# Kernel tuning notes

Hardware: AMD Instinct MI355X
Metric: run time of the kernel (lower is better)

Reference implementation:

```python
import jax, jax.numpy as jnp
import numpy as np

N = 4
IS_SLOW = (False, False, True, True)
RATES = (1, 1, 4, 4)
THRESH = 0.3
F2S_IDX = {(0, 2): 0, (0, 3): 1, (1, 2): 2, (1, 3): 3}


def _conv1d(x, w, stride, pad):
    # x: [B, C_in, T], w: [C_out, C_in, K]
    return jax.lax.conv_general_dilated(
        x, w, (stride,), [(pad, pad)], dimension_numbers=("NCH", "OIH", "NCH"))


def _linear_interp(x, t_out):
    # x: [B, D, T_in] -> [B, D, t_out]; matches F.interpolate(mode='linear', align_corners=False)
    t_in = x.shape[2]
    scale = t_in / t_out
    src = (jnp.arange(t_out, dtype=jnp.float32) + 0.5) * scale - 0.5
    src = jnp.clip(src, 0.0, float(t_in - 1))
    i0 = jnp.floor(src).astype(jnp.int32)
    i1 = jnp.minimum(i0 + 1, t_in - 1)
    w = (src - i0.astype(jnp.float32)).astype(x.dtype)
    return x[:, :, i0] * (1.0 - w) + x[:, :, i1] * w


def setup_inputs() -> dict:
    key = jax.random.key(0)
    ks = jax.random.split(key, 8)
    T_FAST, T_SLOW, B, D, H = 512, 128, 32, 1024, 256
    return {
        "feat0": jax.random.normal(ks[0], (T_FAST, B, D), jnp.float32),
        "feat1": jax.random.normal(ks[1], (T_FAST, B, D), jnp.float32),
        "feat2": jax.random.normal(ks[2], (T_SLOW, B, D), jnp.float32),
        "feat3": jax.random.normal(ks[3], (T_SLOW, B, D), jnp.float32),
        "mlp_w1": jax.random.normal(ks[4], (N * N, 2 * D, H), jnp.float32) * 0.02,
        "mlp_b1": jnp.zeros((N * N, H), jnp.float32),
        "mlp_w2": jax.random.normal(ks[5], (N * N, H, 1), jnp.float32) * 0.02,
        "mlp_b2": jnp.zeros((N * N, 1), jnp.float32),
        "s2f_w": jax.random.normal(ks[6], (D, D, 1), jnp.float32) * 0.02,
        "s2f_b": jnp.zeros((D,), jnp.float32),
        "f2s_w": jax.random.normal(ks[7], (4, D, D, 5), jnp.float32) * 0.02,
    }


def reference(feat0, feat1, feat2, feat3, mlp_w1, mlp_b1, mlp_w2, mlp_b2,
              s2f_w, s2f_b, f2s_w):
    feats = [feat0, feat1, feat2, feat3]            # [T_i, B, D]
    feats_bdt = [jnp.transpose(f, (1, 2, 0)) for f in feats]  # [B, D, T_i]
    globals_ = [f.mean(axis=2) for f in feats_bdt]  # [B, D]
    outputs = list(feats)
    for i in range(N):
        for j in range(N):
            if i == j:
                continue
            p = i * N + j
            pair_vec = jnp.concatenate([globals_[i], globals_[j]], axis=-1)  # [B, 2D]
            h = jax.nn.relu(pair_vec @ mlp_w1[p] + mlp_b1[p])
            score = jax.nn.sigmoid(h @ mlp_w2[p] + mlp_b2[p])[:, 0]          # [B]
            cond = score.mean() >= THRESH
            if IS_SLOW[i] and not IS_SLOW[j]:
                # slow -> fast: interpolate up, 1x1 conv proj, score-weighted residual
                up = _linear_interp(feats_bdt[i], feats_bdt[j].shape[2])
                up = _conv1d(up, s2f_w, 1, 0) + s2f_b[None, :, None]
                new = feats_bdt[j] + score[:, None, None] * up
                outputs[j] = jnp.where(cond, jnp.transpose(new, (2, 0, 1)), outputs[j])
            elif (not IS_SLOW[i]) and IS_SLOW[j]:
                # fast -> slow: strided conv down, score-weighted residual
                stride = RATES[j] // RATES[i]
                down = _conv1d(feats_bdt[i], f2s_w[F2S_IDX[(i, j)]], stride, 2)
                new = feats_bdt[j] + score[:, None, None] * down
                outputs[j] = jnp.where(cond, jnp.transpose(new, (2, 0, 1)), outputs[j])
    return tuple(outputs)
```

## Files before the change

### kernel.cpp

```cpp
#include <hip/hip_runtime.h>
#include <math.h>
#include <stdint.h>

typedef __bf16 bf16;
typedef bf16 bf16x8 __attribute__((ext_vector_type(8)));
typedef bf16 bf16x4 __attribute__((ext_vector_type(4)));
typedef float f32x4 __attribute__((ext_vector_type(4)));

#define OFF_GLOB   0ul
#define OFF_H      524288ul
#define OFF_SCORE  786432ul
#define OFF_COND   787456ul
#define OFF_PART   788480ul
#define OFF_PROJ   4982784ul
#define OFF_WTF2S  38537216ul
#define OFF_WTS2F  59508736ul
#define OFF_F0B    61605888ul
#define OFF_F1B    95160320ul
#define OFF_F2B    128714752ul
#define OFF_F3B    137103360ul
#define WS_NEED    145491968ul

__device__ __forceinline__ void gl2lds16(const void* g, void* lds) {
  __builtin_amdgcn_global_load_lds(
      (const __attribute__((address_space(1))) unsigned int*)g,
      (__attribute__((address_space(3))) unsigned int*)lds, 16, 0, 0);
}

__device__ __forceinline__ void slot_ij(int s, int& i, int& j) {
  if (s < 4) { i = 2 + (s & 1); j = s >> 1; }
  else       { int ss = s - 4; i = ss & 1; j = 2 + (ss >> 1); }
}

__global__ __launch_bounds__(256) void k_means_part(
    const float* __restrict__ f0, const float* __restrict__ f1,
    const float* __restrict__ f2, const float* __restrict__ f3,
    float* __restrict__ part,
    bf16* __restrict__ b0, bf16* __restrict__ b1,
    bf16* __restrict__ b2, bf16* __restrict__ b3, int do_conv)
{
  int b = blockIdx.x, c = blockIdx.y, i = blockIdx.z, tid = threadIdx.x;
  const float* f = (i == 0) ? f0 : (i == 1) ? f1 : (i == 2) ? f2 : f3;
  bf16* fb = (i == 0) ? b0 : (i == 1) ? b1 : (i == 2) ? b2 : b3;
  int chunk = (i < 2) ? 64 : 16;
  int t0 = c * chunk;
  float4 s = make_float4(0.f, 0.f, 0.f, 0.f);
  for (int t = t0; t < t0 + chunk; ++t) {
    float4 v = ((const float4*)(f + (size_t)(t * 32 + b) * 1024))[tid];
    s.x += v.x; s.y += v.y; s.z += v.z; s.w += v.w;
    if (do_conv) {
      bf16x4 o;
      o[0] = (bf16)v.x; o[1] = (bf16)v.y; o[2] = (bf16)v.z; o[3] = (bf16)v.w;
      *(bf16x4*)(fb + (size_t)(t * 32 + b) * 1024 + tid * 4) = o;
    }
  }
  ((float4*)part)[(size_t)((i * 8 + c) * 32 + b) * 256 + tid] = s;
}

__global__ __launch_bounds__(256) void k_means_final(
    const float* __restrict__ part, float* __restrict__ g)
{
  int b = blockIdx.x, i = blockIdx.y, tid = threadIdx.x;
  float4 s = make_float4(0.f, 0.f, 0.f, 0.f);
  for (int c = 0; c < 8; ++c) {
    float4 v = ((const float4*)part)[(size_t)((i * 8 + c) * 32 + b) * 256 + tid];
    s.x += v.x; s.y += v.y; s.z += v.z; s.w += v.w;
  }
  float inv = (i < 2) ? (1.f / 512.f) : (1.f / 128.f);
  s.x *= inv; s.y *= inv; s.z *= inv; s.w *= inv;
  ((float4*)g)[(size_t)(i * 32 + b) * 256 + tid] = s;
}

__global__ __launch_bounds__(256) void k_mlp1(
    const float* __restrict__ g, const float* __restrict__ w1, float* __restrict__ h_ws)
{
  int s = blockIdx.x, hc = blockIdx.y, kz = blockIdx.z, tid = threadIdx.x;
  int pi, pj; slot_ij(s, pi, pj);
  int p = pi * 4 + pj;
  int h = hc * 32 + (tid & 31);
  int bg = tid >> 5;
  __shared__ float pv[32 * 65];
  float acc0 = 0.f, acc1 = 0.f, acc2 = 0.f, acc3 = 0.f;
  for (int kt = 0; kt < 8; ++kt) {
    int k0 = kz * 512 + kt * 64;
    __syncthreads();
    for (int l = tid; l < 2048; l += 256) {
      int bb = l >> 6, kk = l & 63;
      int k = k0 + kk;
      float v = (k < 1024) ? g[(size_t)pi * 32768 + bb * 1024 + k]
                           : g[(size_t)pj * 32768 + bb * 1024 + (k - 1024)];
      pv[bb * 65 + kk] = v;
    }
    __syncthreads();
    const float* wp = w1 + ((size_t)p * 2048 + k0) * 256 + hc * 32 + (tid & 31);
    for (int kk = 0; kk < 64; ++kk) {
      float w = wp[(size_t)kk * 256];
      acc0 += pv[(bg * 4 + 0) * 65 + kk] * w;
      acc1 += pv[(bg * 4 + 1) * 65 + kk] * w;
      acc2 += pv[(bg * 4 + 2) * 65 + kk] * w;
      acc3 += pv[(bg * 4 + 3) * 65 + kk] * w;
    }
  }
  atomicAdd(&h_ws[(size_t)s * 8192 + (bg * 4 + 0) * 256 + h], acc0);
  atomicAdd(&h_ws[(size_t)s * 8192 + (bg * 4 + 1) * 256 + h], acc1);
  atomicAdd(&h_ws[(size_t)s * 8192 + (bg * 4 + 2) * 256 + h], acc2);
  atomicAdd(&h_ws[(size_t)s * 8192 + (bg * 4 + 3) * 256 + h], acc3);
}

__global__ __launch_bounds__(256) void k_mlp2(
    const float* __restrict__ h_ws, const float* __restrict__ b1,
    const float* __restrict__ w2, const float* __restrict__ b2,
    float* __restrict__ score, float* __restrict__ cond)
{
  int s = blockIdx.x, tid = threadIdx.x;
  int pi, pj; slot_ij(s, pi, pj);
  int p = pi * 4 + pj;
  int lane = tid & 63, wv = tid >> 6;
  float4 w2v = ((const float4*)(w2 + p * 256))[lane];
  float4 b1v = ((const float4*)(b1 + p * 256))[lane];
  float b2v = b2[p];
  __shared__ float redw[4];
  float tot = 0.f;
  for (int bb = 0; bb < 8; ++bb) {
    int b = wv * 8 + bb;
    float4 h4 = ((const float4*)(h_ws + (size_t)s * 8192 + b * 256))[lane];
    float v = fmaxf(h4.x + b1v.x, 0.f) * w2v.x + fmaxf(h4.y + b1v.y, 0.f) * w2v.y
            + fmaxf(h4.z + b1v.z, 0.f) * w2v.z + fmaxf(h4.w + b1v.w, 0.f) * w2v.w;
    #pragma unroll
    for (int off = 32; off > 0; off >>= 1) v += __shfl_down(v, off);
    if (lane == 0) {
      float sc = 1.f / (1.f + expf(-(v + b2v)));
      score[s * 32 + b] = sc;
      tot += sc;
    }
  }
  if (lane == 0) redw[wv] = tot;
  __syncthreads();
  if (tid == 0) {
    float t = redw[0] + redw[1] + redw[2] + redw[3];
    cond[s] = (t * (1.f / 32.f) >= 0.3f) ? 1.f : 0.f;
  }
}

__global__ __launch_bounds__(256) void k_f2s_transpose(
    const float* __restrict__ w, const float* __restrict__ cond, bf16* __restrict__ wT)
{
  int z = blockIdx.y, co = blockIdx.x, tid = threadIdx.x;
  int sel = (cond[5 + 2 * z] > 0.5f) ? 1 : ((cond[4 + 2 * z] > 0.5f) ? 0 : -1);
  if (sel < 0) return;
  int widx = sel * 2 + z;
  __shared__ float buf[5120];
  const float* src = w + ((size_t)widx * 1024 + co) * 5120;
  for (int l = tid; l < 5120; l += 256) buf[l] = src[l];
  __syncthreads();
  bf16* dst = wT + (size_t)z * 5242880 + (size_t)co * 5120;
  for (int o = tid; o < 5120; o += 256) {
    int kk = o >> 10, ci = o & 1023;
    dst[o] = (bf16)buf[ci * 5 + kk];
  }
}

__global__ __launch_bounds__(256) void k_s2f_convert(
    const float* __restrict__ w, bf16* __restrict__ wT)
{
  size_t gi = (size_t)blockIdx.x * 256 + threadIdx.x;
  float4 v = ((const float4*)w)[gi];
  bf16x4 o;
  o[0] = (bf16)v.x; o[1] = (bf16)v.y; o[2] = (bf16)v.z; o[3] = (bf16)v.w;
  *(bf16x4*)&wT[gi * 4] = o;
}


__global__ __launch_bounds__(256) void k_s2f_gemm2(
    const bf16* __restrict__ f2b, const bf16* __restrict__ f3b,
    const bf16* __restrict__ wT, const float* __restrict__ s2f_b,
    const float* __restrict__ cond, float* __restrict__ proj)
{
  int z = blockIdx.z;
  int sel = (cond[1 + 2 * z] > 0.5f) ? 3 : ((cond[2 * z] > 0.5f) ? 2 : -1);
  if (sel < 0) return;
  const bf16* Ab = (sel == 3) ? f3b : f2b;
  float* projz = proj + (size_t)z * 4194304;
  int tid = threadIdx.x;
  int lin = blockIdx.y * 32 + blockIdx.x;
  int o_ = (lin & 7) * 32 + (lin >> 3);
  int M0 = (o_ & 31) * 128, N0 = (o_ >> 5) * 128;
  __shared__ bf16 As[2][8192];
  __shared__ bf16 Bs[2][8192];
  f32x4 acc[4][4];
  #pragma unroll
  for (int a = 0; a < 4; ++a)
    #pragma unroll
    for (int c = 0; c < 4; ++c) { acc[a][c][0] = 0.f; acc[a][c][1] = 0.f; acc[a][c][2] = 0.f; acc[a][c][3] = 0.f; }
  int lane = tid & 63, wv = tid >> 6;
  int wr = (wv >> 1) * 64, wc = (wv & 1) * 64;
  int rl = lane & 15, q = lane >> 4;
  int wb = tid & 192;

  size_t aoffs[4], boffs[4];
  #pragma unroll
  for (int rnd = 0; rnd < 4; ++rnd) {
    int c = rnd * 256 + tid, lr = c >> 3, seg = c & 7, sw = seg ^ (lr & 7);
    aoffs[rnd] = (size_t)(M0 + lr) * 1024 + sw * 8;
    boffs[rnd] = (size_t)(N0 + lr) * 1024 + sw * 8;
  }

  #define S2F_STAGE(KT, PB) {                                        \
    size_t ci0 = (size_t)(KT) * 64;                                  \
    _Pragma("unroll")                                                \
    for (int rnd = 0; rnd < 4; ++rnd) {                              \
      gl2lds16(Ab + aoffs[rnd] + ci0, &As[PB][(rnd * 256 + wb) * 8]);\
      gl2lds16(wT + boffs[rnd] + ci0, &Bs[PB][(rnd * 256 + wb) * 8]);\
    } }

  S2F_STAGE(0, 0);
  __syncthreads();
  for (int kt = 0; kt < 16; ++kt) {
    int pb = kt & 1;
    if (kt < 15) S2F_STAGE(kt + 1, pb ^ 1);
    const bf16* Ac = &As[pb][0];
    const bf16* Bc = &Bs[pb][0];
    #pragma unroll
    for (int ks = 0; ks < 2; ++ks) {
      bf16x8 af[4], bfv[4];
      #pragma unroll
      for (int mi = 0; mi < 4; ++mi) {
        int r = wr + mi * 16 + rl;
        af[mi] = *(const bf16x8*)&Ac[r * 64 + (((ks << 2) + q) ^ (r & 7)) * 8];
      }
      #pragma unroll
      for (int ni = 0; ni < 4; ++ni) {
        int r = wc + ni * 16 + rl;
        bfv[ni] = *(const bf16x8*)&Bc[r * 64 + (((ks << 2) + q) ^ (r & 7)) * 8];
      }
      #pragma unroll
      for (int mi = 0; mi < 4; ++mi)
        #pragma unroll
        for (int ni = 0; ni < 4; ++ni)
          acc[mi][ni] = __builtin_amdgcn_mfma_f32_16x16x32_bf16(af[mi], bfv[ni], acc[mi][ni], 0, 0, 0);
    }
    __syncthreads();
  }
  #pragma unroll
  for (int mi = 0; mi < 4; ++mi)
    #pragma unroll
    for (int ni = 0; ni < 4; ++ni)
      #pragma unroll
      for (int r = 0; r < 4; ++r) {
        int gm = M0 + wr + mi * 16 + q * 4 + r;
        int gn = N0 + wc + ni * 16 + rl;
        projz[(size_t)gm * 1024 + gn] = acc[mi][ni][r] + s2f_b[gn];
      }
}

__global__ __launch_bounds__(256) void k_f2s_gemm2(
    const bf16* __restrict__ f0b, const bf16* __restrict__ f1b,
    const float* __restrict__ feat2, const float* __restrict__ feat3,
    const bf16* __restrict__ wT, const float* __restrict__ score,
    const float* __restrict__ cond, const bf16* __restrict__ zbuf,
    float* __restrict__ out)
{
  int z = blockIdx.z;
  const float* fj = z ? feat3 : feat2;
  float* oj = out + 33554432ul + (size_t)z * 4194304;
  int tid = threadIdx.x;
  int lin = blockIdx.y * 32 + blockIdx.x;
  int o_ = (lin & 7) * 32 + (lin >> 3);
  int M0 = (o_ & 31) * 128, N0 = (o_ >> 5) * 128;
  int sel = (cond[5 + 2 * z] > 0.5f) ? 1 : ((cond[4 + 2 * z] > 0.5f) ? 0 : -1);
  if (sel < 0) {
    for (int l = tid; l < 4096; l += 256) {
      int rr = l >> 5, c4 = l & 31;
      size_t idx = (size_t)(M0 + rr) * 1024 + N0 + c4 * 4;
      *(float4*)(oj + idx) = *(const float4*)(fj + idx);
    }
    return;
  }
  const bf16* Ab = sel ? f1b : f0b;
  const bf16* wTz = wT + (size_t)z * 5242880;
  int slot = (sel ? 5 : 4) + 2 * z;
  __shared__ bf16 As[2][8192];
  __shared__ bf16 Bs[2][8192];
  __shared__ float sld[32];
  if (tid < 32) sld[tid] = score[slot * 32 + tid];
  f32x4 acc[4][4];
  #pragma unroll
  for (int a = 0; a < 4; ++a)
    #pragma unroll
    for (int c = 0; c < 4; ++c) { acc[a][c][0] = 0.f; acc[a][c][1] = 0.f; acc[a][c][2] = 0.f; acc[a][c][3] = 0.f; }
  int lane = tid & 63, wv = tid >> 6;
  int wr = (wv >> 1) * 64, wc = (wv & 1) * 64;
  int rl = lane & 15, q = lane >> 4;
  int wb = tid & 192;

  long aoffs[4]; size_t boffs[4]; bool t0f[4];
  #pragma unroll
  for (int rnd = 0; rnd < 4; ++rnd) {
    int c = rnd * 256 + tid, lr = c >> 3, seg = c & 7, sw = seg ^ (lr & 7);
    int m = M0 + lr, t = m >> 5, b = m & 31;
    aoffs[rnd] = ((long)(4 * t - 2) * 32 + b) * 1024 + sw * 8;
    t0f[rnd] = (t == 0);
    boffs[rnd] = (size_t)(N0 + lr) * 5120 + sw * 8;
  }

  #define F2S_STAGE(KT, PB) {                                                   \
    int kk_ = (KT) >> 4;                                                        \
    long aadd_ = (long)kk_ * 32768 + (((KT) & 15) << 6);                        \
    size_t badd_ = (size_t)(KT) * 64;                                           \
    bool zk_ = (kk_ < 2);                                                       \
    _Pragma("unroll")                                                           \
    for (int rnd = 0; rnd < 4; ++rnd) {                                         \
      const bf16* sA = (zk_ && t0f[rnd]) ? zbuf : (Ab + aoffs[rnd] + aadd_);    \
      gl2lds16(sA, &As[PB][(rnd * 256 + wb) * 8]);                              \
      gl2lds16(wTz + boffs[rnd] + badd_, &Bs[PB][(rnd * 256 + wb) * 8]);        \
    } }

  F2S_STAGE(0, 0);
  __syncthreads();
  for (int kt = 0; kt < 80; ++kt) {
    int pb = kt & 1;
    if (kt < 79) F2S_STAGE(kt + 1, pb ^ 1);
    const bf16* Ac = &As[pb][0];
    const bf16* Bc = &Bs[pb][0];
    #pragma unroll
    for (int ks = 0; ks < 2; ++ks) {
      bf16x8 af[4], bfv[4];
      #pragma unroll
      for (int mi = 0; mi < 4; ++mi) {
        int r = wr + mi * 16 + rl;
        af[mi] = *(const bf16x8*)&Ac[r * 64 + (((ks << 2) + q) ^ (r & 7)) * 8];
      }
      #pragma unroll
      for (int ni = 0; ni < 4; ++ni) {
        int r = wc + ni * 16 + rl;
        bfv[ni] = *(const bf16x8*)&Bc[r * 64 + (((ks << 2) + q) ^ (r & 7)) * 8];
      }
      #pragma unroll
      for (int mi = 0; mi < 4; ++mi)
        #pragma unroll
        for (int ni = 0; ni < 4; ++ni)
          acc[mi][ni] = __builtin_amdgcn_mfma_f32_16x16x32_bf16(af[mi], bfv[ni], acc[mi][ni], 0, 0, 0);
    }
    __syncthreads();
  }
  #pragma unroll
  for (int mi = 0; mi < 4; ++mi)
    #pragma unroll
    for (int ni = 0; ni < 4; ++ni)
      #pragma unroll
      for (int r = 0; r < 4; ++r) {
        int gm = M0 + wr + mi * 16 + q * 4 + r;
        int gn = N0 + wc + ni * 16 + rl;
        size_t idx = (size_t)gm * 1024 + gn;
        oj[idx] = fj[idx] + sld[gm & 31] * acc[mi][ni][r];
      }
}

__global__ __launch_bounds__(256) void k_s2f_gemm_fb(
    const float* __restrict__ feat2, const float* __restrict__ feat3,
    const bf16* __restrict__ wT, const float* __restrict__ s2f_b,
    const float* __restrict__ cond, float* __restrict__ proj)
{
  int z = blockIdx.z;
  int sel = (cond[1 + 2 * z] > 0.5f) ? 3 : ((cond[2 * z] > 0.5f) ? 2 : -1);
  if (sel < 0) return;
  const float* A = (sel == 3) ? feat3 : feat2;
  float* projz = proj + (size_t)z * 4194304;
  int tid = threadIdx.x;
  int lin = blockIdx.y * 32 + blockIdx.x;
  int o_ = (lin & 7) * 32 + (lin >> 3);
  int M0 = (o_ & 31) * 128, N0 = (o_ >> 5) * 128;
  __shared__ bf16 As[128][72];
  __shared__ bf16 Bs[128][72];
  f32x4 acc[4][4];
  for (int a = 0; a < 4; ++a)
    for (int c = 0; c < 4; ++c) { acc[a][c][0] = 0.f; acc[a][c][1] = 0.f; acc[a][c][2] = 0.f; acc[a][c][3] = 0.f; }
  int row = tid >> 1, half = tid & 1;
  int lane = tid & 63, wv = tid >> 6;
  int wr = (wv >> 1) * 64, wc = (wv & 1) * 64;
  int rl = lane & 15, q = lane >> 4;
  for (int kt = 0; kt < 16; ++kt) {
    int ci0 = kt * 64;
    __syncthreads();
    {
      const float4* src = (const float4*)(A + (size_t)(M0 + row) * 1024 + ci0 + half * 32);
      #pragma unroll
      for (int u = 0; u < 4; ++u) {
        float4 v0 = src[2 * u], v1 = src[2 * u + 1];
        bf16x8 pk;
        pk[0] = (bf16)v0.x; pk[1] = (bf16)v0.y; pk[2] = (bf16)v0.z; pk[3] = (bf16)v0.w;
        pk[4] = (bf16)v1.x; pk[5] = (bf16)v1.y; pk[6] = (bf16)v1.z; pk[7] = (bf16)v1.w;
        *(bf16x8*)&As[row][half * 32 + u * 8] = pk;
      }
      const uint4* bs = (const uint4*)(wT + (size_t)(N0 + row) * 1024 + ci0 + half * 32);
      #pragma unroll
      for (int u = 0; u < 4; ++u) *(uint4*)&Bs[row][half * 32 + u * 8] = bs[u];
    }
    __syncthreads();
    #pragma unroll
    for (int ks = 0; ks < 2; ++ks) {
      bf16x8 af[4], bfv[4];
      #pragma unroll
      for (int mi = 0; mi < 4; ++mi) af[mi] = *(const bf16x8*)&As[wr + mi * 16 + rl][ks * 32 + q * 8];
      #pragma unroll
      for (int ni = 0; ni < 4; ++ni) bfv[ni] = *(const bf16x8*)&Bs[wc + ni * 16 + rl][ks * 32 + q * 8];
      #pragma unroll
      for (int mi = 0; mi < 4; ++mi)
        #pragma unroll
        for (int ni = 0; ni < 4; ++ni)
          acc[mi][ni] = __builtin_amdgcn_mfma_f32_16x16x32_bf16(af[mi], bfv[ni], acc[mi][ni], 0, 0, 0);
    }
  }
  #pragma unroll
  for (int mi = 0; mi < 4; ++mi)
    #pragma unroll
    for (int ni = 0; ni < 4; ++ni)
      #pragma unroll
      for (int r = 0; r < 4; ++r) {
        int gm = M0 + wr + mi * 16 + q * 4 + r;
        int gn = N0 + wc + ni * 16 + rl;
        projz[(size_t)gm * 1024 + gn] = acc[mi][ni][r] + s2f_b[gn];
      }
}

__global__ __launch_bounds__(256) void k_f2s_gemm_fb(
    const float* __restrict__ feat0, const float* __restrict__ feat1,
    const float* __restrict__ feat2, const float* __restrict__ feat3,
    const bf16* __restrict__ wT, const float* __restrict__ score,
    const float* __restrict__ cond, float* __restrict__ out)
{
  int z = blockIdx.z;
  const float* fj = z ? feat3 : feat2;
  float* oj = out + 33554432ul + (size_t)z * 4194304;
  int tid = threadIdx.x;
  int lin = blockIdx.y * 32 + blockIdx.x;
  int o_ = (lin & 7) * 32 + (lin >> 3);
  int M0 = (o_ & 31) * 128, N0 = (o_ >> 5) * 128;
  int sel = (cond[5 + 2 * z] > 0.5f) ? 1 : ((cond[4 + 2 * z] > 0.5f) ? 0 : -1);
  if (sel < 0) {
    for (int l = tid; l < 4096; l += 256) {
      int rr = l >> 5, c4 = l & 31;
      size_t idx = (size_t)(M0 + rr) * 1024 + N0 + c4 * 4;
      *(float4*)(oj + idx) = *(const float4*)(fj + idx);
    }
    return;
  }
  const float* A = sel ? feat1 : feat0;
  const bf16* wTz = wT + (size_t)z * 5242880;
  int slot = (sel ? 5 : 4) + 2 * z;
  __shared__ bf16 As[128][72];
  __shared__ bf16 Bs[128][72];
  __shared__ float sld[32];
  if (tid < 32) sld[tid] = score[slot * 32 + tid];
  f32x4 acc[4][4];
  for (int a = 0; a < 4; ++a)
    for (int c = 0; c < 4; ++c) { acc[a][c][0] = 0.f; acc[a][c][1] = 0.f; acc[a][c][2] = 0.f; acc[a][c][3] = 0.f; }
  int row = tid >> 1, half = tid & 1;
  int m = M0 + row, t = m >> 5, b = m & 31;
  int lane = tid & 63, wv = tid >> 6;
  int wr = (wv >> 1) * 64, wc = (wv & 1) * 64;
  int rl = lane & 15, q = lane >> 4;
  for (int kt = 0; kt < 80; ++kt) {
    int kk = kt >> 4, ci0 = (kt & 15) << 6;
    int pos = 4 * t - 2 + kk;
    __syncthreads();
    {
      float4 v[8];
      if (pos >= 0 && pos < 512) {
        const float4* src = (const float4*)(A + (size_t)(pos * 32 + b) * 1024 + ci0 + half * 32);
        #pragma unroll
        for (int u = 0; u < 8; ++u) v[u] = src[u];
      } else {
        #pragma unroll
        for (int u = 0; u < 8; ++u) v[u] = make_float4(0.f, 0.f, 0.f, 0.f);
      }
      #pragma unroll
      for (int u = 0; u < 4; ++u) {
        bf16x8 pk;
        pk[0] = (bf16)v[2 * u].x; pk[1] = (bf16)v[2 * u].y; pk[2] = (bf16)v[2 * u].z; pk[3] = (bf16)v[2 * u].w;
        pk[4] = (bf16)v[2 * u + 1].x; pk[5] = (bf16)v[2 * u + 1].y; pk[6] = (bf16)v[2 * u + 1].z; pk[7] = (bf16)v[2 * u + 1].w;
        *(bf16x8*)&As[row][half * 32 + u * 8] = pk;
      }
      const uint4* bs = (const uint4*)(wTz + (size_t)(N0 + row) * 5120 + kt * 64 + half * 32);
      #pragma unroll
      for (int u = 0; u < 4; ++u) *(uint4*)&Bs[row][half * 32 + u * 8] = bs[u];
    }
    __syncthreads();
    #pragma unroll
    for (int ks = 0; ks < 2; ++ks) {
      bf16x8 af[4], bfv[4];
      #pragma unroll
      for (int mi = 0; mi < 4; ++mi) af[mi] = *(const bf16x8*)&As[wr + mi * 16 + rl][ks * 32 + q * 8];
      #pragma unroll
      for (int ni = 0; ni < 4; ++ni) bfv[ni] = *(const bf16x8*)&Bs[wc + ni * 16 + rl][ks * 32 + q * 8];
      #pragma unroll
      for (int mi = 0; mi < 4; ++mi)
        #pragma unroll
        for (int ni = 0; ni < 4; ++ni)
          acc[mi][ni] = __builtin_amdgcn_mfma_f32_16x16x32_bf16(af[mi], bfv[ni], acc[mi][ni], 0, 0, 0);
    }
  }
  #pragma unroll
  for (int mi = 0; mi < 4; ++mi)
    #pragma unroll
    for (int ni = 0; ni < 4; ++ni)
      #pragma unroll
      for (int r = 0; r < 4; ++r) {
        int gm = M0 + wr + mi * 16 + q * 4 + r;
        int gn = N0 + wc + ni * 16 + rl;
        size_t idx = (size_t)gm * 1024 + gn;
        oj[idx] = fj[idx] + sld[gm & 31] * acc[mi][ni][r];
      }
}

__global__ __launch_bounds__(256) void k_interp(
    const float* __restrict__ f0, const float* __restrict__ f1,
    const float* __restrict__ proj, const float* __restrict__ score,
    const float* __restrict__ cond, float* __restrict__ out)
{
  int z = blockIdx.y, tb = blockIdx.x, tid = threadIdx.x;
  const float* fj = z ? f1 : f0;
  float* oj = out + (size_t)z * 16777216;
  int sel = (cond[1 + 2 * z] > 0.5f) ? 3 : ((cond[2 * z] > 0.5f) ? 2 : -1);
  float4 fv = ((const float4*)(fj + (size_t)tb * 1024))[tid];
  if (sel < 0) {
    ((float4*)(oj + (size_t)tb * 1024))[tid] = fv;
    return;
  }
  int t = tb >> 5, b = tb & 31;
  int slot = 2 * z + (sel == 3 ? 1 : 0);
  float s = score[slot * 32 + b];
  float srcf = 0.25f * (float)t - 0.375f;
  srcf = fminf(fmaxf(srcf, 0.f), 127.f);
  int i0 = (int)srcf;
  int i1 = min(i0 + 1, 127);
  float w = srcf - (float)i0;
  const float* pz = proj + (size_t)z * 4194304;
  float4 a = ((const float4*)(pz + (size_t)(i0 * 32 + b) * 1024))[tid];
  float4 c = ((const float4*)(pz + (size_t)(i1 * 32 + b) * 1024))[tid];
  float4 o;
  o.x = fv.x + s * ((1.f - w) * a.x + w * c.x);
  o.y = fv.y + s * ((1.f - w) * a.y + w * c.y);
  o.z = fv.z + s * ((1.f - w) * a.z + w * c.z);
  o.w = fv.w + s * ((1.f - w) * a.w + w * c.w);
  ((float4*)(oj + (size_t)tb * 1024))[tid] = o;
}

extern "C" void kernel_launch(void* const* d_in, const int* in_sizes, int n_in,
                              void* d_out, int out_size, void* d_ws, size_t ws_size,
                              hipStream_t stream) {
  const float* f0   = (const float*)d_in[0];
  const float* f1   = (const float*)d_in[1];
  const float* f2   = (const float*)d_in[2];
  const float* f3   = (const float*)d_in[3];
  const float* w1   = (const float*)d_in[4];
  const float* b1   = (const float*)d_in[5];
  const float* w2   = (const float*)d_in[6];
  const float* b2   = (const float*)d_in[7];
  const float* s2fw = (const float*)d_in[8];
  const float* s2fb = (const float*)d_in[9];
  const float* f2sw = (const float*)d_in[10];
  float* out = (float*)d_out;

  char* ws = (char*)d_ws;
  float* g     = (float*)(ws + OFF_GLOB);
  float* h_ws  = (float*)(ws + OFF_H);
  float* score = (float*)(ws + OFF_SCORE);
  float* cond  = (float*)(ws + OFF_COND);
  bf16*  zbuf  = (bf16*)(ws + OFF_COND + 256);
  float* part  = (float*)(ws + OFF_PART);
  float* proj  = (float*)(ws + OFF_PROJ);
  bf16*  wtf   = (bf16*)(ws + OFF_WTF2S);
  bf16*  wts   = (bf16*)(ws + OFF_WTS2F);
  bf16*  f0b   = (bf16*)(ws + OFF_F0B);
  bf16*  f1b   = (bf16*)(ws + OFF_F1B);
  bf16*  f2b   = (bf16*)(ws + OFF_F2B);
  bf16*  f3b   = (bf16*)(ws + OFF_F3B);

  const bool pre = (ws_size >= WS_NEED);

  hipMemsetAsync(h_ws, 0, 262144, stream);
  hipMemsetAsync(ws + OFF_COND + 256, 0, 64, stream);
  if (pre)
    k_means_part<<<dim3(32, 8, 4), 256, 0, stream>>>(f0, f1, f2, f3, part, f0b, f1b, f2b, f3b, 1);
  else
    k_means_part<<<dim3(32, 8, 4), 256, 0, stream>>>(f0, f1, f2, f3, part,
                                                     (bf16*)nullptr, (bf16*)nullptr,
                                                     (bf16*)nullptr, (bf16*)nullptr, 0);
  k_means_final<<<dim3(32, 4), 256, 0, stream>>>(part, g);
  k_mlp1<<<dim3(8, 8, 4), 256, 0, stream>>>(g, w1, h_ws);
  k_mlp2<<<8, 256, 0, stream>>>(h_ws, b1, w2, b2, score, cond);
  k_f2s_transpose<<<dim3(1024, 2), 256, 0, stream>>>(f2sw, cond, wtf);
  k_s2f_convert<<<1024, 256, 0, stream>>>(s2fw, wts);
  if (pre) {
    k_s2f_gemm2<<<dim3(32, 8, 2), 256, 0, stream>>>(f2b, f3b, wts, s2fb, cond, proj);
    k_f2s_gemm2<<<dim3(32, 8, 2), 256, 0, stream>>>(f0b, f1b, f2, f3, wtf, score, cond, zbuf, out);
  } else {
    k_s2f_gemm_fb<<<dim3(32, 8, 2), 256, 0, stream>>>(f2, f3, wts, s2fb, cond, proj);
    k_f2s_gemm_fb<<<dim3(32, 8, 2), 256, 0, stream>>>(f0, f1, f2, f3, wtf, score, cond, out);
  }
  k_interp<<<dim3(16384, 2), 256, 0, stream>>>(f0, f1, proj, score, cond, out);
}
```

Baseline: 626.3 us.

## Merge s2f and f2s GEMMs into one launch with split-K atomic accumulation

Combines the s2f and f2s GEMM kernels into a single launch of 6 z-slices. The 5120-deep f2s reduction is split into two K-halves that atomically add into the output, and k_means_part now pre-copies feat2/feat3 into the output as the residual base. The goal is more parallel blocks and better CU occupancy for the long f2s GEMM, plus one fewer launch. In exchange it drops LDS double buffering (single buffer with two syncs per tile), adds float atomics to the outputs, and makes the f32 summation order nondeterministic.

Result: slower. 643.7 us (+2.8%).

```diff
diff --git a/kernel.cpp b/kernel.cpp
--- a/kernel.cpp
+++ b/kernel.cpp
@@ -37,11 +37,13 @@
     const float* __restrict__ f2, const float* __restrict__ f3,
     float* __restrict__ part,
     bf16* __restrict__ b0, bf16* __restrict__ b1,
-    bf16* __restrict__ b2, bf16* __restrict__ b3, int do_conv)
+    bf16* __restrict__ b2, bf16* __restrict__ b3, int do_conv,
+    float* __restrict__ out)
 {
   int b = blockIdx.x, c = blockIdx.y, i = blockIdx.z, tid = threadIdx.x;
   const float* f = (i == 0) ? f0 : (i == 1) ? f1 : (i == 2) ? f2 : f3;
   bf16* fb = (i == 0) ? b0 : (i == 1) ? b1 : (i == 2) ? b2 : b3;
+  float* pf = (i == 2) ? (out + 33554432ul) : (i == 3) ? (out + 37748736ul) : nullptr;
   int chunk = (i < 2) ? 64 : 16;
   int t0 = c * chunk;
   float4 s = make_float4(0.f, 0.f, 0.f, 0.f);
@@ -53,6 +55,7 @@
       o[0] = (bf16)v.x; o[1] = (bf16)v.y; o[2] = (bf16)v.z; o[3] = (bf16)v.w;
       *(bf16x4*)(fb + (size_t)(t * 32 + b) * 1024 + tid * 4) = o;
     }
+    if (pf) ((float4*)(pf + (size_t)(t * 32 + b) * 1024))[tid] = v;
   }
   ((float4*)part)[(size_t)((i * 8 + c) * 32 + b) * 256 + tid] = s;
 }
@@ -171,189 +174,134 @@
 }
 
 
-__global__ __launch_bounds__(256) void k_s2f_gemm2(
+#define COMPUTE_TILE()                                                           \
+  _Pragma("unroll")                                                              \
+  for (int ks = 0; ks < 2; ++ks) {                                               \
+    bf16x8 af[4], bfv[4];                                                        \
+    _Pragma("unroll")                                                            \
+    for (int mi = 0; mi < 4; ++mi) {                                             \
+      int r = wr + mi * 16 + rl;                                                 \
+      af[mi] = *(const bf16x8*)&As[r * 64 + (((ks << 2) + q) ^ (r & 7)) * 8];    \
+    }                                                                            \
+    _Pragma("unroll")                                                            \
+    for (int ni = 0; ni < 4; ++ni) {                                             \
+      int r = wc + ni * 16 + rl;                                                 \
+      bfv[ni] = *(const bf16x8*)&Bs[r * 64 + (((ks << 2) + q) ^ (r & 7)) * 8];   \
+    }                                                                            \
+    _Pragma("unroll")                                                            \
+    for (int mi = 0; mi < 4; ++mi)                                               \
+      _Pragma("unroll")                                                          \
+      for (int ni = 0; ni < 4; ++ni)                                             \
+        acc[mi][ni] = __builtin_amdgcn_mfma_f32_16x16x32_bf16(af[mi], bfv[ni], acc[mi][ni], 0, 0, 0); \
+  }
+
+__global__ __launch_bounds__(256) void k_gemm_all(
+    const bf16* __restrict__ f0b, const bf16* __restrict__ f1b,
     const bf16* __restrict__ f2b, const bf16* __restrict__ f3b,
-    const bf16* __restrict__ wT, const float* __restrict__ s2f_b,
-    const float* __restrict__ cond, float* __restrict__ proj)
-{
-  int z = blockIdx.z;
-  int sel = (cond[1 + 2 * z] > 0.5f) ? 3 : ((cond[2 * z] > 0.5f) ? 2 : -1);
-  if (sel < 0) return;
-  const bf16* Ab = (sel == 3) ? f3b : f2b;
-  float* projz = proj + (size_t)z * 4194304;
-  int tid = threadIdx.x;
+    const bf16* __restrict__ wtf, const bf16* __restrict__ wts,
+    const float* __restrict__ s2f_b, const float* __restrict__ score,
+    const float* __restrict__ cond, const bf16* __restrict__ zbuf,
+    float* __restrict__ proj, float* __restrict__ out)
+{
+  int z = blockIdx.z, tid = threadIdx.x;
   int lin = blockIdx.y * 32 + blockIdx.x;
   int o_ = (lin & 7) * 32 + (lin >> 3);
   int M0 = (o_ & 31) * 128, N0 = (o_ >> 5) * 128;
-  __shared__ bf16 As[2][8192];
-  __shared__ bf16 Bs[2][8192];
-  f32x4 acc[4][4];
-  #pragma unroll
-  for (int a = 0; a < 4; ++a)
-    #pragma unroll
-    for (int c = 0; c < 4; ++c) { acc[a][c][0] = 0.f; acc[a][c][1] = 0.f; acc[a][c][2] = 0.f; acc[a][c][3] = 0.f; }
   int lane = tid & 63, wv = tid >> 6;
   int wr = (wv >> 1) * 64, wc = (wv & 1) * 64;
   int rl = lane & 15, q = lane >> 4;
   int wb = tid & 192;
 
-  size_t aoffs[4], boffs[4];
-  #pragma unroll
-  for (int rnd = 0; rnd < 4; ++rnd) {
-    int c = rnd * 256 + tid, lr = c >> 3, seg = c & 7, sw = seg ^ (lr & 7);
-    aoffs[rnd] = (size_t)(M0 + lr) * 1024 + sw * 8;
-    boffs[rnd] = (size_t)(N0 + lr) * 1024 + sw * 8;
-  }
-
-  #define S2F_STAGE(KT, PB) {                                        \
-    size_t ci0 = (size_t)(KT) * 64;                                  \
-    _Pragma("unroll")                                                \
-    for (int rnd = 0; rnd < 4; ++rnd) {                              \
-      gl2lds16(Ab + aoffs[rnd] + ci0, &As[PB][(rnd * 256 + wb) * 8]);\
-      gl2lds16(wT + boffs[rnd] + ci0, &Bs[PB][(rnd * 256 + wb) * 8]);\
-    } }
-
-  S2F_STAGE(0, 0);
-  __syncthreads();
-  for (int kt = 0; kt < 16; ++kt) {
-    int pb = kt & 1;
-    if (kt < 15) S2F_STAGE(kt + 1, pb ^ 1);
-    const bf16* Ac = &As[pb][0];
-    const bf16* Bc = &Bs[pb][0];
-    #pragma unroll
-    for (int ks = 0; ks < 2; ++ks) {
-      bf16x8 af[4], bfv[4];
-      #pragma unroll
-      for (int mi = 0; mi < 4; ++mi) {
-        int r = wr + mi * 16 + rl;
-        af[mi] = *(const bf16x8*)&Ac[r * 64 + (((ks << 2) + q) ^ (r & 7)) * 8];
-      }
-      #pragma unroll
-      for (int ni = 0; ni < 4; ++ni) {
-        int r = wc + ni * 16 + rl;
-        bfv[ni] = *(const bf16x8*)&Bc[r * 64 + (((ks << 2) + q) ^ (r & 7)) * 8];
-      }
-      #pragma unroll
-      for (int mi = 0; mi < 4; ++mi)
-        #pragma unroll
-        for (int ni = 0; ni < 4; ++ni)
-          acc[mi][ni] = __builtin_amdgcn_mfma_f32_16x16x32_bf16(af[mi], bfv[ni], acc[mi][ni], 0, 0, 0);
-    }
-    __syncthreads();
-  }
-  #pragma unroll
-  for (int mi = 0; mi < 4; ++mi)
-    #pragma unroll
-    for (int ni = 0; ni < 4; ++ni)
-      #pragma unroll
-      for (int r = 0; r < 4; ++r) {
-        int gm = M0 + wr + mi * 16 + q * 4 + r;
-        int gn = N0 + wc + ni * 16 + rl;
-        projz[(size_t)gm * 1024 + gn] = acc[mi][ni][r] + s2f_b[gn];
-      }
-}
-
-__global__ __launch_bounds__(256) void k_f2s_gemm2(
-    const bf16* __restrict__ f0b, const bf16* __restrict__ f1b,
-    const float* __restrict__ feat2, const float* __restrict__ feat3,
-    const bf16* __restrict__ wT, const float* __restrict__ score,
-    const float* __restrict__ cond, const bf16* __restrict__ zbuf,
-    float* __restrict__ out)
-{
-  int z = blockIdx.z;
-  const float* fj = z ? feat3 : feat2;
-  float* oj = out + 33554432ul + (size_t)z * 4194304;
-  int tid = threadIdx.x;
-  int lin = blockIdx.y * 32 + blockIdx.x;
-  int o_ = (lin & 7) * 32 + (lin >> 3);
-  int M0 = (o_ & 31) * 128, N0 = (o_ >> 5) * 128;
-  int sel = (cond[5 + 2 * z] > 0.5f) ? 1 : ((cond[4 + 2 * z] > 0.5f) ? 0 : -1);
-  if (sel < 0) {
-    for (int l = tid; l < 4096; l += 256) {
-      int rr = l >> 5, c4 = l & 31;
-      size_t idx = (size_t)(M0 + rr) * 1024 + N0 + c4 * 4;
-      *(float4*)(oj + idx) = *(const float4*)(fj + idx);
-    }
-    return;
-  }
-  const bf16* Ab = sel ? f1b : f0b;
-  const bf16* wTz = wT + (size_t)z * 5242880;
-  int slot = (sel ? 5 : 4) + 2 * z;
-  __shared__ bf16 As[2][8192];
-  __shared__ bf16 Bs[2][8192];
+  __shared__ bf16 As[8192];
+  __shared__ bf16 Bs[8192];
   __shared__ float sld[32];
-  if (tid < 32) sld[tid] = score[slot * 32 + tid];
+
   f32x4 acc[4][4];
   #pragma unroll
   for (int a = 0; a < 4; ++a)
     #pragma unroll
     for (int c = 0; c < 4; ++c) { acc[a][c][0] = 0.f; acc[a][c][1] = 0.f; acc[a][c][2] = 0.f; acc[a][c][3] = 0.f; }
-  int lane = tid & 63, wv = tid >> 6;
-  int wr = (wv >> 1) * 64, wc = (wv & 1) * 64;
-  int rl = lane & 15, q = lane >> 4;
-  int wb = tid & 192;
-
-  long aoffs[4]; size_t boffs[4]; bool t0f[4];
-  #pragma unroll
-  for (int rnd = 0; rnd < 4; ++rnd) {
-    int c = rnd * 256 + tid, lr = c >> 3, seg = c & 7, sw = seg ^ (lr & 7);
-    int m = M0 + lr, t = m >> 5, b = m & 31;
-    aoffs[rnd] = ((long)(4 * t - 2) * 32 + b) * 1024 + sw * 8;
-    t0f[rnd] = (t == 0);
-    boffs[rnd] = (size_t)(N0 + lr) * 5120 + sw * 8;
-  }
-
-  #define F2S_STAGE(KT, PB) {                                                   \
-    int kk_ = (KT) >> 4;                                                        \
-    long aadd_ = (long)kk_ * 32768 + (((KT) & 15) << 6);                        \
-    size_t badd_ = (size_t)(KT) * 64;                                           \
-    bool zk_ = (kk_ < 2);                                                       \
-    _Pragma("unroll")                                                           \
-    for (int rnd = 0; rnd < 4; ++rnd) {                                         \
-      const bf16* sA = (zk_ && t0f[rnd]) ? zbuf : (Ab + aoffs[rnd] + aadd_);    \
-      gl2lds16(sA, &As[PB][(rnd * 256 + wb) * 8]);                              \
-      gl2lds16(wTz + boffs[rnd] + badd_, &Bs[PB][(rnd * 256 + wb) * 8]);        \
-    } }
-
-  F2S_STAGE(0, 0);
-  __syncthreads();
-  for (int kt = 0; kt < 80; ++kt) {
-    int pb = kt & 1;
-    if (kt < 79) F2S_STAGE(kt + 1, pb ^ 1);
-    const bf16* Ac = &As[pb][0];
-    const bf16* Bc = &Bs[pb][0];
-    #pragma unroll
-    for (int ks = 0; ks < 2; ++ks) {
-      bf16x8 af[4], bfv[4];
-      #pragma unroll
-      for (int mi = 0; mi < 4; ++mi) {
-        int r = wr + mi * 16 + rl;
-        af[mi] = *(const bf16x8*)&Ac[r * 64 + (((ks << 2) + q) ^ (r & 7)) * 8];
-      }
-      #pragma unroll
-      for (int ni = 0; ni < 4; ++ni) {
-        int r = wc + ni * 16 + rl;
-        bfv[ni] = *(const bf16x8*)&Bc[r * 64 + (((ks << 2) + q) ^ (r & 7)) * 8];
-      }
-      #pragma unroll
-      for (int mi = 0; mi < 4; ++mi)
+
+  if (z < 2) {
+    int sel = (cond[1 + 2 * z] > 0.5f) ? 3 : ((cond[2 * z] > 0.5f) ? 2 : -1);
+    if (sel < 0) return;
+    const bf16* Ab = (sel == 3) ? f3b : f2b;
+    float* projz = proj + (size_t)z * 4194304;
+    size_t aoffs[4], boffs[4];
+    #pragma unroll
+    for (int rnd = 0; rnd < 4; ++rnd) {
+      int c = rnd * 256 + tid, lr = c >> 3, seg = c & 7, sw = seg ^ (lr & 7);
+      aoffs[rnd] = (size_t)(M0 + lr) * 1024 + sw * 8;
+      boffs[rnd] = (size_t)(N0 + lr) * 1024 + sw * 8;
+    }
+    for (int kt = 0; kt < 16; ++kt) {
+      size_t ci0 = (size_t)kt * 64;
+      #pragma unroll
+      for (int rnd = 0; rnd < 4; ++rnd) {
+        gl2lds16(Ab + aoffs[rnd] + ci0, &As[(rnd * 256 + wb) * 8]);
+        gl2lds16(wts + boffs[rnd] + ci0, &Bs[(rnd * 256 + wb) * 8]);
+      }
+      __syncthreads();
+      COMPUTE_TILE();
+      __syncthreads();
+    }
+    #pragma unroll
+    for (int mi = 0; mi < 4; ++mi)
+      #pragma unroll
+      for (int ni = 0; ni < 4; ++ni)
         #pragma unroll
-        for (int ni = 0; ni < 4; ++ni)
-          acc[mi][ni] = __builtin_amdgcn_mfma_f32_16x16x32_bf16(af[mi], bfv[ni], acc[mi][ni], 0, 0, 0);
-    }
-    __syncthreads();
-  }
-  #pragma unroll
-  for (int mi = 0; mi < 4; ++mi)
-    #pragma unroll
-    for (int ni = 0; ni < 4; ++ni)
-      #pragma unroll
-      for (int r = 0; r < 4; ++r) {
-        int gm = M0 + wr + mi * 16 + q * 4 + r;
-        int gn = N0 + wc + ni * 16 + rl;
-        size_t idx = (size_t)gm * 1024 + gn;
-        oj[idx] = fj[idx] + sld[gm & 31] * acc[mi][ni][r];
-      }
+        for (int r = 0; r < 4; ++r) {
+          int gm = M0 + wr + mi * 16 + q * 4 + r;
+          int gn = N0 + wc + ni * 16 + rl;
+          projz[(size_t)gm * 1024 + gn] = acc[mi][ni][r] + s2f_b[gn];
+        }
+  } else {
+    int zf = (z - 2) >> 1, kh = (z - 2) & 1;
+    int sel = (cond[5 + 2 * zf] > 0.5f) ? 1 : ((cond[4 + 2 * zf] > 0.5f) ? 0 : -1);
+    if (sel < 0) return;
+    const bf16* Ab = sel ? f1b : f0b;
+    const bf16* wTz = wtf + (size_t)zf * 5242880;
+    float* oj = out + 33554432ul + (size_t)zf * 4194304;
+    int slot = (sel ? 5 : 4) + 2 * zf;
+    if (tid < 32) sld[tid] = score[slot * 32 + tid];
+    __syncthreads();
+
+    long aoffs[4]; size_t boffs[4]; bool t0f[4];
+    #pragma unroll
+    for (int rnd = 0; rnd < 4; ++rnd) {
+      int c = rnd * 256 + tid, lr = c >> 3, seg = c & 7, sw = seg ^ (lr & 7);
+      int m = M0 + lr, t = m >> 5, b = m & 31;
+      aoffs[rnd] = ((long)(4 * t - 2) * 32 + b) * 1024 + sw * 8;
+      t0f[rnd] = (t == 0);
+      boffs[rnd] = (size_t)(N0 + lr) * 5120 + sw * 8;
+    }
+    int kb = kh * 40;
+    for (int kt = kb; kt < kb + 40; ++kt) {
+      int kk = kt >> 4;
+      long aadd = (long)kk * 32768 + ((kt & 15) << 6);
+      size_t badd = (size_t)kt * 64;
+      bool zk = (kk < 2);
+      #pragma unroll
+      for (int rnd = 0; rnd < 4; ++rnd) {
+        const bf16* sA = (zk && t0f[rnd]) ? zbuf : (Ab + aoffs[rnd] + aadd);
+        gl2lds16(sA, &As[(rnd * 256 + wb) * 8]);
+        gl2lds16(wTz + boffs[rnd] + badd, &Bs[(rnd * 256 + wb) * 8]);
+      }
+      __syncthreads();
+      COMPUTE_TILE();
+      __syncthreads();
+    }
+    #pragma unroll
+    for (int mi = 0; mi < 4; ++mi)
+      #pragma unroll
+      for (int ni = 0; ni < 4; ++ni)
+        #pragma unroll
+        for (int r = 0; r < 4; ++r) {
+          int gm = M0 + wr + mi * 16 + q * 4 + r;
+          int gn = N0 + wc + ni * 16 + rl;
+          atomicAdd(&oj[(size_t)gm * 1024 + gn], sld[gm & 31] * acc[mi][ni][r]);
+        }
+  }
 }
 
 __global__ __launch_bounds__(256) void k_s2f_gemm_fb(
@@ -582,19 +530,19 @@
   hipMemsetAsync(h_ws, 0, 262144, stream);
   hipMemsetAsync(ws + OFF_COND + 256, 0, 64, stream);
   if (pre)
-    k_means_part<<<dim3(32, 8, 4), 256, 0, stream>>>(f0, f1, f2, f3, part, f0b, f1b, f2b, f3b, 1);
+    k_means_part<<<dim3(32, 8, 4), 256, 0, stream>>>(f0, f1, f2, f3, part, f0b, f1b, f2b, f3b, 1, out);
   else
     k_means_part<<<dim3(32, 8, 4), 256, 0, stream>>>(f0, f1, f2, f3, part,
                                                      (bf16*)nullptr, (bf16*)nullptr,
-                                                     (bf16*)nullptr, (bf16*)nullptr, 0);
+                                                     (bf16*)nullptr, (bf16*)nullptr, 0, out);
   k_means_final<<<dim3(32, 4), 256, 0, stream>>>(part, g);
   k_mlp1<<<dim3(8, 8, 4), 256, 0, stream>>>(g, w1, h_ws);
   k_mlp2<<<8, 256, 0, stream>>>(h_ws, b1, w2, b2, score, cond);
   k_f2s_transpose<<<dim3(1024, 2), 256, 0, stream>>>(f2sw, cond, wtf);
   k_s2f_convert<<<1024, 256, 0, stream>>>(s2fw, wts);
   if (pre) {
-    k_s2f_gemm2<<<dim3(32, 8, 2), 256, 0, stream>>>(f2b, f3b, wts, s2fb, cond, proj);
-    k_f2s_gemm2<<<dim3(32, 8, 2), 256, 0, stream>>>(f0b, f1b, f2, f3, wtf, score, cond, zbuf, out);
+    k_gemm_all<<<dim3(32, 8, 6), 256, 0, stream>>>(f0b, f1b, f2b, f3b, wtf, wts, s2fb,
+                                                   score, cond, zbuf, proj, out);
   } else {
     k_s2f_gemm_fb<<<dim3(32, 8, 2), 256, 0, stream>>>(f2, f3, wts, s2fb, cond, proj);
     k_f2s_gemm_fb<<<dim3(32, 8, 2), 256, 0, stream>>>(f0, f1, f2, f3, wtf, score, cond, out);
```
